# Kernel optimization log

Hardware: AMD Instinct MI355X
Metric: run time of the kernel (lower is better)

The kernel has to match this reference:

```python
import jax, jax.numpy as jnp
import numpy as np

LN_EPS = 1e-5
LOG_EPS = 1e-8

def _layernorm(x, w, b):
    mu = jnp.mean(x, axis=-1, keepdims=True)
    var = jnp.mean((x - mu) ** 2, axis=-1, keepdims=True)
    return (x - mu) * jax.lax.rsqrt(var + LN_EPS) * w + b


def setup_inputs() -> dict:
    key = jax.random.key(0)
    ks = jax.random.split(key, 8)
    B, T, D = 4, 4096, 1024
    x = jax.random.normal(ks[0], (B, T, D), dtype=jnp.float32)
    ln_w = jnp.ones((D,), jnp.float32)
    ln_b = jnp.zeros((D,), jnp.float32)
    # torch Linear stores weight as (out, in)
    Wf = jax.random.normal(ks[1], (D, D), jnp.float32) / np.sqrt(D)
    bf = jax.random.normal(ks[2], (D,), jnp.float32) * 0.02
    # module inits reach to zeros; use small random values for a non-trivial baseline
    Wr = jax.random.normal(ks[3], (D, D), jnp.float32) * 0.02
    br = jax.random.normal(ks[4], (D,), jnp.float32) * 0.02
    alpha_bias = jnp.array([3.0], jnp.float32) + jax.random.normal(ks[5], (1,), jnp.float32) * 0.1
    beta_scale = jnp.array([0.02], jnp.float32)
    return {"x": x, "ln_w": ln_w, "ln_b": ln_b, "Wf": Wf, "bf": bf,
            "Wr": Wr, "br": br, "alpha_bias": alpha_bias, "beta_scale": beta_scale}


def reference(x, ln_w, ln_b, Wf, bf, Wr, br, alpha_bias, beta_scale):
    residual = x
    x_norm = _layernorm(x, ln_w, ln_b)                       # [B,T,D]
    alpha = jax.nn.sigmoid(jnp.einsum('btd,ed->bte', x_norm, Wf) + bf + alpha_bias)
    beta_x = beta_scale * (1.0 - alpha) * x_norm
    log_alpha = jnp.log(alpha + LOG_EPS)
    log_alpha_cumsum = jnp.cumsum(log_alpha, axis=1)          # [B,T,D]
    m = jnp.max(log_alpha_cumsum, axis=1, keepdims=True)      # [B,1,D]
    scale = jnp.exp(log_alpha_cumsum - m)
    x_star = beta_x * scale
    s_star = jnp.cumsum(x_star, axis=1)
    output = s_star / (scale + LOG_EPS)
    x_gate = jnp.tanh(jnp.einsum('btd,ed->bte', output, Wr) + br)
    return x_gate * 0.05 + residual
```

## Files before the change

### kernel.cpp

```cpp
#include <hip/hip_runtime.h>

#define D_DIM 1024
#define B_DIM 4
#define T_DIM 4096
#define M_DIM (B_DIM * T_DIM)
#define CHUNK 32
#define NCHUNK (T_DIM / CHUNK)
#define NWAVE_C 16
#define SEG (NCHUNK / NWAVE_C)

typedef unsigned short u16;
typedef __attribute__((ext_vector_type(8))) __bf16 bf16x8;
typedef __attribute__((ext_vector_type(4))) float f32x4;

__device__ __forceinline__ float bf2f(u16 u) {
    union { unsigned int i; float f; } v;
    v.i = ((unsigned int)u) << 16;
    return v.f;
}
__device__ __forceinline__ u16 f2bf(float f) {
    union { float f; unsigned int i; } v;
    v.f = f;
    unsigned int u = v.i;
    unsigned int r = (u + 0x7fffu + ((u >> 16) & 1u)) >> 16;
    return (u16)r;
}
__device__ __forceinline__ float fast_tanh(float v) {
    float e = __expf(2.f * v);
    return 1.f - 2.f / (e + 1.f);
}

#define GLOAD16(g, l)                                                   \
    __builtin_amdgcn_global_load_lds(                                   \
        (const __attribute__((address_space(1))) void*)(g),             \
        (__attribute__((address_space(3))) void*)(l), 16, 0, 0)

__global__ __launch_bounds__(256) void ln_conv_kernel(const float* __restrict__ x,
                                                      const float* __restrict__ w,
                                                      const float* __restrict__ b,
                                                      u16* __restrict__ xn,
                                                      const float* __restrict__ Wf,
                                                      const float* __restrict__ Wr,
                                                      u16* __restrict__ da,
                                                      u16* __restrict__ db) {
    int tid = threadIdx.x;
    if (blockIdx.x < 2048) {
        int i = blockIdx.x * 256 + tid;
        const float* s = (i < 262144) ? Wf : Wr;
        u16* dp = (i < 262144) ? da : db;
        int j = i & 262143;
        float4 v = ((const float4*)s)[j];
        ushort4 o;
        o.x = f2bf(v.x); o.y = f2bf(v.y); o.z = f2bf(v.z); o.w = f2bf(v.w);
        ((ushort4*)dp)[j] = o;
        return;
    }
    int wv = tid >> 6, lane = tid & 63;
    int row = (blockIdx.x - 2048) * 4 + wv;
    const float4* xr = (const float4*)(x + (size_t)row * D_DIM);
    float4 xv[4];
    #pragma unroll
    for (int k = 0; k < 4; k++) xv[k] = xr[lane + 64 * k];
    float s = 0.f, s2 = 0.f;
    #pragma unroll
    for (int k = 0; k < 4; k++) {
        s  += xv[k].x + xv[k].y + xv[k].z + xv[k].w;
        s2 += xv[k].x * xv[k].x + xv[k].y * xv[k].y
            + xv[k].z * xv[k].z + xv[k].w * xv[k].w;
    }
    #pragma unroll
    for (int o = 1; o < 64; o <<= 1) {
        s  += __shfl_xor(s, o, 64);
        s2 += __shfl_xor(s2, o, 64);
    }
    float mu = s * (1.0f / D_DIM);
    float var = s2 * (1.0f / D_DIM) - mu * mu;
    float rs = rsqrtf(var + 1e-5f);
    ushort4* xo = (ushort4*)(xn + (size_t)row * D_DIM);
    #pragma unroll
    for (int k = 0; k < 4; k++) {
        float4 wv4 = ((const float4*)w)[lane + 64 * k];
        float4 bv4 = ((const float4*)b)[lane + 64 * k];
        ushort4 o;
        o.x = f2bf((xv[k].x - mu) * rs * wv4.x + bv4.x);
        o.y = f2bf((xv[k].y - mu) * rs * wv4.y + bv4.y);
        o.z = f2bf((xv[k].z - mu) * rs * wv4.z + bv4.z);
        o.w = f2bf((xv[k].w - mu) * rs * wv4.w + bv4.w);
        xo[lane + 64 * k] = o;
    }
}

__global__ __launch_bounds__(256) void gemm1_kernel(const u16* __restrict__ xn,
                                                    const u16* __restrict__ Wfc,
                                                    const float* __restrict__ bf_,
                                                    const float* __restrict__ ab,
                                                    const float* __restrict__ bs,
                                                    u16* __restrict__ out_la,
                                                    float* __restrict__ Sg,
                                                    float* __restrict__ Tg) {
    __shared__ __align__(16) u16 lds_a[128 * 32];
    __shared__ __align__(16) u16 lds_b[128 * 32];
    int tid  = threadIdx.x;
    int wave = tid >> 6, lane = tid & 63;
    int tile_n = blockIdx.x * 128;
    int tile_m = blockIdx.y * 128;
    int wr = wave >> 1, wc = wave & 1;
    f32x4 acc[4][4] = {};

    int srow = wave * 32 + (lane >> 2);
    int scol = (lane & 3) * 8;
    const u16* ga0 = xn  + (size_t)(tile_m + srow) * D_DIM + scol;
    const u16* ga1 = ga0 + 16 * D_DIM;
    const u16* gb0 = Wfc + (size_t)(tile_n + srow) * D_DIM + scol;
    const u16* gb1 = gb0 + 16 * D_DIM;
    u16* la0 = &lds_a[(wave * 32) * 32];
    u16* la1 = &lds_a[(wave * 32 + 16) * 32];
    u16* lb0 = &lds_b[(wave * 32) * 32];
    u16* lb1 = &lds_b[(wave * 32 + 16) * 32];

    for (int k0 = 0; k0 < D_DIM; k0 += 32) {
        GLOAD16(ga0 + k0, la0);
        GLOAD16(ga1 + k0, la1);
        GLOAD16(gb0 + k0, lb0);
        GLOAD16(gb1 + k0, lb1);
        __syncthreads();
        bf16x8 af[4], bfr[4];
        #pragma unroll
        for (int mi = 0; mi < 4; mi++) {
            int m = wr * 64 + mi * 16 + (lane & 15);
            af[mi] = *(const bf16x8*)&lds_a[m * 32 + (lane >> 4) * 8];
        }
        #pragma unroll
        for (int ni = 0; ni < 4; ni++) {
            int n = wc * 64 + ni * 16 + (lane & 15);
            bfr[ni] = *(const bf16x8*)&lds_b[n * 32 + (lane >> 4) * 8];
        }
        #pragma unroll
        for (int mi = 0; mi < 4; mi++)
            #pragma unroll
            for (int ni = 0; ni < 4; ni++)
                acc[mi][ni] = __builtin_amdgcn_mfma_f32_16x16x32_bf16(
                    af[mi], bfr[ni], acc[mi][ni], 0, 0, 0);
        __syncthreads();
    }

    float abv = ab[0], bsv = bs[0];
    int q = lane >> 4, l = lane & 15;
    #pragma unroll
    for (int ni = 0; ni < 4; ni++) {
        int col = tile_n + wc * 64 + ni * 16 + l;
        float bcol = bf_[col];
        #pragma unroll
        for (int ch = 0; ch < 2; ch++) {
            float lav[2][4], bxv[2][4];
            #pragma unroll
            for (int h = 0; h < 2; h++) {
                int mi = 2 * ch + h;
                #pragma unroll
                for (int r = 0; r < 4; r++) {
                    int row = tile_m + wr * 64 + mi * 16 + q * 4 + r;
                    float z = acc[mi][ni][r] + bcol + abv;
                    float alpha = 1.f / (1.f + __expf(-z));
                    float la_ = __logf(alpha + 1e-8f);
                    float xv = bf2f(xn[(size_t)row * D_DIM + col]);
                    lav[h][r] = la_;
                    bxv[h][r] = bsv * (1.f - alpha) * xv;
                    out_la[(size_t)row * D_DIM + col] = f2bf(la_);
                }
            }
            float s0 = lav[0][0] + lav[0][1] + lav[0][2] + lav[0][3];
            float s1 = lav[1][0] + lav[1][1] + lav[1][2] + lav[1][3];
            float x0 = s0, x1 = s1, y;
            y = __shfl_up(x0, 16, 64); if (q >= 1) x0 += y;
            y = __shfl_up(x0, 32, 64); if (q >= 2) x0 += y;
            y = __shfl_up(x1, 16, 64); if (q >= 1) x1 += y;
            y = __shfl_up(x1, 32, 64); if (q >= 2) x1 += y;
            float t0 = __shfl(x0, l + 48, 64);
            float t1 = __shfl(x1, l + 48, 64);
            float e0 = x0 - s0, e1 = x1 - s1;
            float pr = e0, Tp = 0.f;
            #pragma unroll
            for (int r = 0; r < 4; r++) { pr += lav[0][r]; Tp += bxv[0][r] * __expf(pr); }
            pr = t0 + e1;
            #pragma unroll
            for (int r = 0; r < 4; r++) { pr += lav[1][r]; Tp += bxv[1][r] * __expf(pr); }
            Tp += __shfl_xor(Tp, 16, 64);
            Tp += __shfl_xor(Tp, 32, 64);
            if (q == 0) {
                int cidx = (tile_m >> 5) + wr * 2 + ch;
                Sg[(size_t)cidx * D_DIM + col] = t0 + t1;
                Tg[(size_t)cidx * D_DIM + col] = Tp;
            }
        }
    }
}

__global__ __launch_bounds__(1024) void scan_combine(const u16* __restrict__ la,
                                                     const float* __restrict__ S,
                                                     const float* __restrict__ Tb,
                                                     float* __restrict__ Of,
                                                     float* __restrict__ SSp) {
    __shared__ float lsS[NWAVE_C][64], lsW[NWAVE_C][64];
    int b = blockIdx.x >> 4;
    int dg = blockIdx.x & 15;
    int wave = threadIdx.x >> 6, lane = threadIdx.x & 63;
    int d = dg * 64 + lane;
    float m = bf2f(la[(size_t)(b * T_DIM) * D_DIM + d]);
    size_t base = ((size_t)b * NCHUNK) * D_DIM + d;
    int c0 = wave * SEG;

    float OfR[SEG], wR[SEG];
    float Or = 0.f, w = 0.f;
    #pragma unroll
    for (int j = 0; j < SEG; j++) {
        size_t ci = base + (size_t)(c0 + j) * D_DIM;
        OfR[j] = Or;
        wR[j]  = w;
        w  += __expf(Or) * Tb[ci];
        Or += S[ci];
    }
    lsS[wave][lane] = Or; lsW[wave][lane] = w;
    __syncthreads();

    float o = 0.f, s = 0.f, myO = 0.f, myS = 0.f;
    #pragma unroll
    for (int w2 = 0; w2 < NWAVE_C; w2++) {
        if (w2 == wave) { myO = o; myS = s; }
        s += __expf(o - m) * lsW[w2][lane];
        o += lsS[w2][lane];
    }

    float em = __expf(myO - m);
    #pragma unroll
    for (int j = 0; j < SEG; j++) {
        size_t ci = base + (size_t)(c0 + j) * D_DIM;
        Of[ci]  = myO + OfR[j] - m;
        SSp[ci] = myS + em * wR[j];
    }
}

__global__ __launch_bounds__(256) void scan_final(const u16* __restrict__ la,
                                                  const u16* __restrict__ xn,
                                                  const float* __restrict__ bs,
                                                  const float* __restrict__ Of,
                                                  const float* __restrict__ SSp,
                                                  u16* __restrict__ osc) {
    int bc = blockIdx.x;
    int b = bc >> 7, c = bc & (NCHUNK - 1);
    int col0 = threadIdx.x * 4;
    float bsv = bs[0];
    size_t base = ((size_t)(b * T_DIM + c * CHUNK)) * D_DIM + col0;
    size_t ci = ((size_t)(b * NCHUNK + c)) * D_DIM + col0;
    float ofs[4], ss[4], p[4];
    #pragma unroll
    for (int j = 0; j < 4; j++) { ofs[j] = Of[ci + j]; ss[j] = SSp[ci + j]; p[j] = 0.f; }
    #pragma unroll 8
    for (int t = 0; t < CHUNK; t++) {
        size_t idx = base + (size_t)t * D_DIM;
        ushort4 lv = *(const ushort4*)(la + idx);
        ushort4 xv = *(const ushort4*)(xn + idx);
        u16 lvs[4] = {lv.x, lv.y, lv.z, lv.w};
        u16 xvs[4] = {xv.x, xv.y, xv.z, xv.w};
        u16 os[4];
        #pragma unroll
        for (int j = 0; j < 4; j++) {
            float lav = bf2f(lvs[j]);
            p[j] += lav;
            float scv = __expf(ofs[j] + p[j]);
            float bx = bsv * (1.f - __expf(lav)) * bf2f(xvs[j]);
            ss[j] += bx * scv;
            os[j] = f2bf(ss[j] / (scv + 1e-8f));
        }
        ushort4 o; o.x = os[0]; o.y = os[1]; o.z = os[2]; o.w = os[3];
        *(ushort4*)(osc + idx) = o;
    }
}

__global__ __launch_bounds__(256) void gemm2_kernel(const u16* __restrict__ A,
                                                    const u16* __restrict__ Bm,
                                                    const float* __restrict__ bias,
                                                    const float* __restrict__ resid,
                                                    float* __restrict__ out_f) {
    __shared__ __align__(16) u16 lds_a[128 * 32];
    __shared__ __align__(16) u16 lds_b[128 * 32];
    int tid  = threadIdx.x;
    int wave = tid >> 6, lane = tid & 63;
    int tile_n = blockIdx.x * 128;
    int tile_m = blockIdx.y * 128;
    int wr = wave >> 1, wc = wave & 1;
    f32x4 acc[4][4] = {};
    int srow = wave * 32 + (lane >> 2);
    int scol = (lane & 3) * 8;
    const u16* ga0 = A  + (size_t)(tile_m + srow) * D_DIM + scol;
    const u16* ga1 = ga0 + 16 * D_DIM;
    const u16* gb0 = Bm + (size_t)(tile_n + srow) * D_DIM + scol;
    const u16* gb1 = gb0 + 16 * D_DIM;
    u16* la0 = &lds_a[(wave * 32) * 32];
    u16* la1 = &lds_a[(wave * 32 + 16) * 32];
    u16* lb0 = &lds_b[(wave * 32) * 32];
    u16* lb1 = &lds_b[(wave * 32 + 16) * 32];
    for (int k0 = 0; k0 < D_DIM; k0 += 32) {
        GLOAD16(ga0 + k0, la0);
        GLOAD16(ga1 + k0, la1);
        GLOAD16(gb0 + k0, lb0);
        GLOAD16(gb1 + k0, lb1);
        __syncthreads();
        bf16x8 af[4], bfr[4];
        #pragma unroll
        for (int mi = 0; mi < 4; mi++) {
            int m = wr * 64 + mi * 16 + (lane & 15);
            af[mi] = *(const bf16x8*)&lds_a[m * 32 + (lane >> 4) * 8];
        }
        #pragma unroll
        for (int ni = 0; ni < 4; ni++) {
            int n = wc * 64 + ni * 16 + (lane & 15);
            bfr[ni] = *(const bf16x8*)&lds_b[n * 32 + (lane >> 4) * 8];
        }
        #pragma unroll
        for (int mi = 0; mi < 4; mi++)
            #pragma unroll
            for (int ni = 0; ni < 4; ni++)
                acc[mi][ni] = __builtin_amdgcn_mfma_f32_16x16x32_bf16(
                    af[mi], bfr[ni], acc[mi][ni], 0, 0, 0);
        __syncthreads();
    }
    #pragma unroll
    for (int mi = 0; mi < 4; mi++) {
        #pragma unroll
        for (int r = 0; r < 4; r++) {
            int row = tile_m + wr * 64 + mi * 16 + (lane >> 4) * 4 + r;
            #pragma unroll
            for (int ni = 0; ni < 4; ni++) {
                int col = tile_n + wc * 64 + ni * 16 + (lane & 15);
                size_t idx = (size_t)row * D_DIM + col;
                float g = fast_tanh(acc[mi][ni][r] + bias[col]);
                out_f[idx] = 0.05f * g + resid[idx];
            }
        }
    }
}

extern "C" void kernel_launch(void* const* d_in, const int* in_sizes, int n_in,
                              void* d_out, int out_size, void* d_ws, size_t ws_size,
                              hipStream_t stream) {
    const float* x   = (const float*)d_in[0];
    const float* lnw = (const float*)d_in[1];
    const float* lnb = (const float*)d_in[2];
    const float* Wf  = (const float*)d_in[3];
    const float* bf_ = (const float*)d_in[4];
    const float* Wr  = (const float*)d_in[5];
    const float* br  = (const float*)d_in[6];
    const float* ab  = (const float*)d_in[7];
    const float* bs  = (const float*)d_in[8];
    float* out = (float*)d_out;

    char* w = (char*)d_ws;
    u16* xn  = (u16*)w;
    u16* la  = (u16*)(w + (size_t)33554432);
    u16* Wfc = (u16*)(w + (size_t)67108864);
    u16* Wrc = (u16*)(w + (size_t)69206016);
    float* S   = (float*)(w + (size_t)71303168);
    float* Tb  = S  + 524288;
    float* Of  = Tb + 524288;
    float* SSp = Of + 524288;
    u16* osc = xn;

    ln_conv_kernel<<<dim3(2048 + M_DIM / 4), dim3(256), 0, stream>>>(
        x, lnw, lnb, xn, Wf, Wr, Wfc, Wrc);
    gemm1_kernel<<<dim3(D_DIM / 128, M_DIM / 128), dim3(256), 0, stream>>>(
        xn, Wfc, bf_, ab, bs, la, S, Tb);
    scan_combine<<<dim3(B_DIM * 16), dim3(1024), 0, stream>>>(la, S, Tb, Of, SSp);
    scan_final<<<dim3(B_DIM * NCHUNK), dim3(256), 0, stream>>>(la, xn, bs, Of, SSp, osc);
    gemm2_kernel<<<dim3(D_DIM / 128, M_DIM / 128), dim3(256), 0, stream>>>(
        osc, Wrc, br, x, out);
}
```

Before: 293.8 us.

## Double-buffer LDS staging in both GEMMs and remap blocks per XCD

Both GEMM kernels now use two LDS buffers so the global-to-LDS loads for the next K-slice are issued while MFMAs run on the current slice, halving the barriers per K step. Block indices are also remapped so each XCD gets a contiguous band of M tiles covering all N tiles, which should improve L2 reuse of the A rows. LDS use per block doubles, which may lower occupancy, and the remap assumes an 8-wide by 128-tall grid.

```diff
diff --git a/kernel.cpp b/kernel.cpp
--- a/kernel.cpp
+++ b/kernel.cpp
@@ -98,12 +98,14 @@
                                                     u16* __restrict__ out_la,
                                                     float* __restrict__ Sg,
                                                     float* __restrict__ Tg) {
-    __shared__ __align__(16) u16 lds_a[128 * 32];
-    __shared__ __align__(16) u16 lds_b[128 * 32];
+    __shared__ __align__(16) u16 lds_a[2][128 * 32];
+    __shared__ __align__(16) u16 lds_b[2][128 * 32];
     int tid  = threadIdx.x;
     int wave = tid >> 6, lane = tid & 63;
-    int tile_n = blockIdx.x * 128;
-    int tile_m = blockIdx.y * 128;
+    int flat = blockIdx.y * 8 + blockIdx.x;
+    int xcd = flat & 7, p = flat >> 3;
+    int tile_m = (xcd * 16 + (p >> 3)) * 128;
+    int tile_n = (p & 7) * 128;
     int wr = wave >> 1, wc = wave & 1;
     f32x4 acc[4][4] = {};
 
@@ -113,36 +115,46 @@
     const u16* ga1 = ga0 + 16 * D_DIM;
     const u16* gb0 = Wfc + (size_t)(tile_n + srow) * D_DIM + scol;
     const u16* gb1 = gb0 + 16 * D_DIM;
-    u16* la0 = &lds_a[(wave * 32) * 32];
-    u16* la1 = &lds_a[(wave * 32 + 16) * 32];
-    u16* lb0 = &lds_b[(wave * 32) * 32];
-    u16* lb1 = &lds_b[(wave * 32 + 16) * 32];
-
-    for (int k0 = 0; k0 < D_DIM; k0 += 32) {
-        GLOAD16(ga0 + k0, la0);
-        GLOAD16(ga1 + k0, la1);
-        GLOAD16(gb0 + k0, lb0);
-        GLOAD16(gb1 + k0, lb1);
+    u16* lA0 = &lds_a[0][(wave * 32) * 32];
+    u16* lA1 = &lds_a[0][(wave * 32 + 16) * 32];
+    u16* lB0 = &lds_b[0][(wave * 32) * 32];
+    u16* lB1 = &lds_b[0][(wave * 32 + 16) * 32];
+
+#define STAGE_G(bufi, kk)                         \
+    do {                                          \
+        GLOAD16(ga0 + (kk), lA0 + (bufi) * 4096); \
+        GLOAD16(ga1 + (kk), lA1 + (bufi) * 4096); \
+        GLOAD16(gb0 + (kk), lB0 + (bufi) * 4096); \
+        GLOAD16(gb1 + (kk), lB1 + (bufi) * 4096); \
+    } while (0)
+
+#define COMPUTE_G(bufi)                                                                      \
+    do {                                                                                     \
+        bf16x8 af[4], bfr[4];                                                                \
+        _Pragma("unroll") for (int mi = 0; mi < 4; mi++)                                     \
+            af[mi] = *(const bf16x8*)&lds_a[bufi][(wr * 64 + mi * 16 + (lane & 15)) * 32 +   \
+                                                  (lane >> 4) * 8];                          \
+        _Pragma("unroll") for (int ni = 0; ni < 4; ni++)                                     \
+            bfr[ni] = *(const bf16x8*)&lds_b[bufi][(wc * 64 + ni * 16 + (lane & 15)) * 32 +  \
+                                                   (lane >> 4) * 8];                         \
+        _Pragma("unroll") for (int mi = 0; mi < 4; mi++)                                     \
+            _Pragma("unroll") for (int ni = 0; ni < 4; ni++)                                 \
+                acc[mi][ni] = __builtin_amdgcn_mfma_f32_16x16x32_bf16(                       \
+                    af[mi], bfr[ni], acc[mi][ni], 0, 0, 0);                                  \
+    } while (0)
+
+    STAGE_G(0, 0);
+    __syncthreads();
+    for (int k0 = 0; k0 < D_DIM; k0 += 64) {
+        STAGE_G(1, k0 + 32);
+        COMPUTE_G(0);
         __syncthreads();
-        bf16x8 af[4], bfr[4];
-        #pragma unroll
-        for (int mi = 0; mi < 4; mi++) {
-            int m = wr * 64 + mi * 16 + (lane & 15);
-            af[mi] = *(const bf16x8*)&lds_a[m * 32 + (lane >> 4) * 8];
-        }
-        #pragma unroll
-        for (int ni = 0; ni < 4; ni++) {
-            int n = wc * 64 + ni * 16 + (lane & 15);
-            bfr[ni] = *(const bf16x8*)&lds_b[n * 32 + (lane >> 4) * 8];
-        }
-        #pragma unroll
-        for (int mi = 0; mi < 4; mi++)
-            #pragma unroll
-            for (int ni = 0; ni < 4; ni++)
-                acc[mi][ni] = __builtin_amdgcn_mfma_f32_16x16x32_bf16(
-                    af[mi], bfr[ni], acc[mi][ni], 0, 0, 0);
+        if (k0 + 64 < D_DIM) STAGE_G(0, k0 + 64);
+        COMPUTE_G(1);
         __syncthreads();
     }
+#undef STAGE_G
+#undef COMPUTE_G
 
     float abv = ab[0], bsv = bs[0];
     int q = lane >> 4, l = lane & 15;
@@ -281,12 +293,14 @@
                                                     const float* __restrict__ bias,
                                                     const float* __restrict__ resid,
                                                     float* __restrict__ out_f) {
-    __shared__ __align__(16) u16 lds_a[128 * 32];
-    __shared__ __align__(16) u16 lds_b[128 * 32];
+    __shared__ __align__(16) u16 lds_a[2][128 * 32];
+    __shared__ __align__(16) u16 lds_b[2][128 * 32];
     int tid  = threadIdx.x;
     int wave = tid >> 6, lane = tid & 63;
-    int tile_n = blockIdx.x * 128;
-    int tile_m = blockIdx.y * 128;
+    int flat = blockIdx.y * 8 + blockIdx.x;
+    int xcd = flat & 7, p = flat >> 3;
+    int tile_m = (xcd * 16 + (p >> 3)) * 128;
+    int tile_n = (p & 7) * 128;
     int wr = wave >> 1, wc = wave & 1;
     f32x4 acc[4][4] = {};
     int srow = wave * 32 + (lane >> 2);
@@ -295,35 +309,47 @@
     const u16* ga1 = ga0 + 16 * D_DIM;
     const u16* gb0 = Bm + (size_t)(tile_n + srow) * D_DIM + scol;
     const u16* gb1 = gb0 + 16 * D_DIM;
-    u16* la0 = &lds_a[(wave * 32) * 32];
-    u16* la1 = &lds_a[(wave * 32 + 16) * 32];
-    u16* lb0 = &lds_b[(wave * 32) * 32];
-    u16* lb1 = &lds_b[(wave * 32 + 16) * 32];
-    for (int k0 = 0; k0 < D_DIM; k0 += 32) {
-        GLOAD16(ga0 + k0, la0);
-        GLOAD16(ga1 + k0, la1);
-        GLOAD16(gb0 + k0, lb0);
-        GLOAD16(gb1 + k0, lb1);
+    u16* lA0 = &lds_a[0][(wave * 32) * 32];
+    u16* lA1 = &lds_a[0][(wave * 32 + 16) * 32];
+    u16* lB0 = &lds_b[0][(wave * 32) * 32];
+    u16* lB1 = &lds_b[0][(wave * 32 + 16) * 32];
+
+#define STAGE_G(bufi, kk)                         \
+    do {                                          \
+        GLOAD16(ga0 + (kk), lA0 + (bufi) * 4096); \
+        GLOAD16(ga1 + (kk), lA1 + (bufi) * 4096); \
+        GLOAD16(gb0 + (kk), lB0 + (bufi) * 4096); \
+        GLOAD16(gb1 + (kk), lB1 + (bufi) * 4096); \
+    } while (0)
+
+#define COMPUTE_G(bufi)                                                                      \
+    do {                                                                                     \
+        bf16x8 af[4], bfr[4];                                                                \
+        _Pragma("unroll") for (int mi = 0; mi < 4; mi++)                                     \
+            af[mi] = *(const bf16x8*)&lds_a[bufi][(wr * 64 + mi * 16 + (lane & 15)) * 32 +   \
+                                                  (lane >> 4) * 8];                          \
+        _Pragma("unroll") for (int ni = 0; ni < 4; ni++)                                     \
+            bfr[ni] = *(const bf16x8*)&lds_b[bufi][(wc * 64 + ni * 16 + (lane & 15)) * 32 +  \
+                                                   (lane >> 4) * 8];                         \
+        _Pragma("unroll") for (int mi = 0; mi < 4; mi++)                                     \
+            _Pragma("unroll") for (int ni = 0; ni < 4; ni++)                                 \
+                acc[mi][ni] = __builtin_amdgcn_mfma_f32_16x16x32_bf16(                       \
+                    af[mi], bfr[ni], acc[mi][ni], 0, 0, 0);                                  \
+    } while (0)
+
+    STAGE_G(0, 0);
+    __syncthreads();
+    for (int k0 = 0; k0 < D_DIM; k0 += 64) {
+        STAGE_G(1, k0 + 32);
+        COMPUTE_G(0);
         __syncthreads();
-        bf16x8 af[4], bfr[4];
-        #pragma unroll
-        for (int mi = 0; mi < 4; mi++) {
-            int m = wr * 64 + mi * 16 + (lane & 15);
-            af[mi] = *(const bf16x8*)&lds_a[m * 32 + (lane >> 4) * 8];
-        }
-        #pragma unroll
-        for (int ni = 0; ni < 4; ni++) {
-            int n = wc * 64 + ni * 16 + (lane & 15);
-            bfr[ni] = *(const bf16x8*)&lds_b[n * 32 + (lane >> 4) * 8];
-        }
-        #pragma unroll
-        for (int mi = 0; mi < 4; mi++)
-            #pragma unroll
-            for (int ni = 0; ni < 4; ni++)
-                acc[mi][ni] = __builtin_amdgcn_mfma_f32_16x16x32_bf16(
-                    af[mi], bfr[ni], acc[mi][ni], 0, 0, 0);
+        if (k0 + 64 < D_DIM) STAGE_G(0, k0 + 64);
+        COMPUTE_G(1);
         __syncthreads();
     }
+#undef STAGE_G
+#undef COMPUTE_G
+
     #pragma unroll
     for (int mi = 0; mi < 4; mi++) {
         #pragma unroll
```

New measurement: 295.7 us. Within noise of the previous version (+0.7%).

## Rewrite both GEMMs with 256x256 tiles, double-buffered swizzled LDS and XCD-aware mapping

Applied to the files above, without the earlier changes.

Both GEMM kernels now share a core that uses 256x256 output tiles with 512 threads and a 64-wide K step. Global-to-LDS loads are double-buffered with explicit vmcnt waits and barriers, the LDS layout is XOR-swizzled to avoid bank conflicts, and MFMA batches run at raised priority. Blocks are remapped so neighbouring tiles land on the same XCD for L2 reuse. The aim is higher MFMA utilisation and less load latency exposure, at the cost of more registers and LDS per block (128KB), which lowers occupancy and leaves only 256 blocks per GEMM.

```diff
diff --git a/kernel.cpp b/kernel.cpp
--- a/kernel.cpp
+++ b/kernel.cpp
@@ -8,6 +8,7 @@
 #define NCHUNK (T_DIM / CHUNK)
 #define NWAVE_C 16
 #define SEG (NCHUNK / NWAVE_C)
+#define NKT (D_DIM / 64)
 
 typedef unsigned short u16;
 typedef __attribute__((ext_vector_type(8))) __bf16 bf16x8;
@@ -34,6 +35,17 @@
     __builtin_amdgcn_global_load_lds(                                   \
         (const __attribute__((address_space(1))) void*)(g),             \
         (__attribute__((address_space(3))) void*)(l), 16, 0, 0)
+
+#define BAR()                                      \
+    do {                                           \
+        __builtin_amdgcn_sched_barrier(0);         \
+        asm volatile("" ::: "memory");             \
+        __builtin_amdgcn_s_barrier();              \
+        asm volatile("" ::: "memory");             \
+        __builtin_amdgcn_sched_barrier(0);         \
+    } while (0)
+
+#define WAITVM(N) asm volatile("s_waitcnt vmcnt(" #N ")" ::: "memory")
 
 __global__ __launch_bounds__(256) void ln_conv_kernel(const float* __restrict__ x,
                                                       const float* __restrict__ w,
@@ -90,60 +102,119 @@
     }
 }
 
-__global__ __launch_bounds__(256) void gemm1_kernel(const u16* __restrict__ xn,
-                                                    const u16* __restrict__ Wfc,
-                                                    const float* __restrict__ bf_,
-                                                    const float* __restrict__ ab,
-                                                    const float* __restrict__ bs,
-                                                    u16* __restrict__ out_la,
-                                                    float* __restrict__ Sg,
-                                                    float* __restrict__ Tg) {
-    __shared__ __align__(16) u16 lds_a[128 * 32];
-    __shared__ __align__(16) u16 lds_b[128 * 32];
+__device__ __forceinline__ void gemm256_core(const u16* __restrict__ AG,
+                                             const u16* __restrict__ BG,
+                                             int tile_m, int tile_n,
+                                             u16* ldsA, u16* ldsB,
+                                             f32x4 (*acc)[4]) {
     int tid  = threadIdx.x;
     int wave = tid >> 6, lane = tid & 63;
-    int tile_n = blockIdx.x * 128;
-    int tile_m = blockIdx.y * 128;
-    int wr = wave >> 1, wc = wave & 1;
-    f32x4 acc[4][4] = {};
-
-    int srow = wave * 32 + (lane >> 2);
-    int scol = (lane & 3) * 8;
-    const u16* ga0 = xn  + (size_t)(tile_m + srow) * D_DIM + scol;
-    const u16* ga1 = ga0 + 16 * D_DIM;
-    const u16* gb0 = Wfc + (size_t)(tile_n + srow) * D_DIM + scol;
-    const u16* gb1 = gb0 + 16 * D_DIM;
-    u16* la0 = &lds_a[(wave * 32) * 32];
-    u16* la1 = &lds_a[(wave * 32 + 16) * 32];
-    u16* lb0 = &lds_b[(wave * 32) * 32];
-    u16* lb1 = &lds_b[(wave * 32 + 16) * 32];
-
-    for (int k0 = 0; k0 < D_DIM; k0 += 32) {
-        GLOAD16(ga0 + k0, la0);
-        GLOAD16(ga1 + k0, la1);
-        GLOAD16(gb0 + k0, lb0);
-        GLOAD16(gb1 + k0, lb1);
-        __syncthreads();
-        bf16x8 af[4], bfr[4];
+    int wr = wave >> 2, wc = wave & 3;
+    int q = lane >> 4;
+    int srow = tid >> 3;
+    int scol = ((tid & 7) ^ (srow & 7)) * 8;
+    const u16* gA = AG + (size_t)(tile_m + srow) * D_DIM + scol;
+    const u16* gB = BG + (size_t)(tile_n + srow) * D_DIM + scol;
+    int ldst = wave * 512;
+    int aRow = wr * 128 + (lane & 15);
+    int bRow = wc * 64 + (lane & 15);
+    int x7 = lane & 7;
+    int s0 = (q ^ x7) * 8;
+    int s1 = ((4 | q) ^ x7) * 8;
+
+#define STG4(ldsbase, gsrc, koff)                                        \
+    do {                                                                 \
+        _Pragma("unroll") for (int j = 0; j < 4; j++)                    \
+            GLOAD16((gsrc) + (size_t)j * (64 * D_DIM) + (koff),          \
+                    (ldsbase) + j * 4096 + ldst);                        \
+    } while (0)
+
+#define MMQ(Af, Bf, mo, no)                                              \
+    do {                                                                 \
+        __builtin_amdgcn_s_setprio(1);                                   \
+        _Pragma("unroll") for (int mi_ = 0; mi_ < 4; mi_++)              \
+            _Pragma("unroll") for (int ni_ = 0; ni_ < 2; ni_++) {        \
+                acc[(mo) + mi_][(no) + ni_] =                            \
+                    __builtin_amdgcn_mfma_f32_16x16x32_bf16(             \
+                        Af[mi_][0], Bf[ni_][0],                          \
+                        acc[(mo) + mi_][(no) + ni_], 0, 0, 0);           \
+                acc[(mo) + mi_][(no) + ni_] =                            \
+                    __builtin_amdgcn_mfma_f32_16x16x32_bf16(             \
+                        Af[mi_][1], Bf[ni_][1],                          \
+                        acc[(mo) + mi_][(no) + ni_], 0, 0, 0);           \
+            }                                                            \
+        __builtin_amdgcn_s_setprio(0);                                   \
+    } while (0)
+
+    STG4(ldsA, gA, 0);
+    STG4(ldsB, gB, 0);
+    STG4(ldsA + 16384, gA, 64);
+    STG4(ldsB + 16384, gB, 64);
+    WAITVM(8);
+    BAR();
+
+    for (int t = 0; t < NKT; t++) {
+        int c = t & 1;
+        const u16* pA = ldsA + c * 16384 + aRow * 64;
+        const u16* pB = ldsB + c * 16384 + bRow * 64;
+        bf16x8 A0[4][2], A1[4][2], B0[2][2], B1[2][2];
         #pragma unroll
         for (int mi = 0; mi < 4; mi++) {
-            int m = wr * 64 + mi * 16 + (lane & 15);
-            af[mi] = *(const bf16x8*)&lds_a[m * 32 + (lane >> 4) * 8];
-        }
-        #pragma unroll
-        for (int ni = 0; ni < 4; ni++) {
-            int n = wc * 64 + ni * 16 + (lane & 15);
-            bfr[ni] = *(const bf16x8*)&lds_b[n * 32 + (lane >> 4) * 8];
-        }
-        #pragma unroll
-        for (int mi = 0; mi < 4; mi++)
-            #pragma unroll
-            for (int ni = 0; ni < 4; ni++)
-                acc[mi][ni] = __builtin_amdgcn_mfma_f32_16x16x32_bf16(
-                    af[mi], bfr[ni], acc[mi][ni], 0, 0, 0);
-        __syncthreads();
-    }
-
+            A0[mi][0] = *(const bf16x8*)(pA + mi * 1024 + s0);
+            A0[mi][1] = *(const bf16x8*)(pA + mi * 1024 + s1);
+        }
+        #pragma unroll
+        for (int ni = 0; ni < 2; ni++) {
+            B0[ni][0] = *(const bf16x8*)(pB + ni * 1024 + s0);
+            B0[ni][1] = *(const bf16x8*)(pB + ni * 1024 + s1);
+        }
+        MMQ(A0, B0, 0, 0);
+        #pragma unroll
+        for (int mi = 0; mi < 4; mi++) {
+            A1[mi][0] = *(const bf16x8*)(pA + (mi + 4) * 1024 + s0);
+            A1[mi][1] = *(const bf16x8*)(pA + (mi + 4) * 1024 + s1);
+        }
+        #pragma unroll
+        for (int ni = 0; ni < 2; ni++) {
+            B1[ni][0] = *(const bf16x8*)(pB + (ni + 2) * 1024 + s0);
+            B1[ni][1] = *(const bf16x8*)(pB + (ni + 2) * 1024 + s1);
+        }
+        MMQ(A0, B1, 0, 2);
+        BAR();
+        if (t + 2 < NKT) STG4(ldsA + c * 16384, gA, (size_t)(t + 2) * 64);
+        MMQ(A1, B0, 4, 0);
+        if (t + 2 < NKT) {
+            STG4(ldsB + c * 16384, gB, (size_t)(t + 2) * 64);
+            WAITVM(8);
+        } else {
+            WAITVM(0);
+        }
+        BAR();
+        MMQ(A1, B1, 4, 2);
+    }
+#undef STG4
+#undef MMQ
+}
+
+__global__ __launch_bounds__(512, 2) void gemm1_kernel(const u16* __restrict__ xn,
+                                                       const u16* __restrict__ Wfc,
+                                                       const float* __restrict__ bf_,
+                                                       const float* __restrict__ ab,
+                                                       const float* __restrict__ bs,
+                                                       u16* __restrict__ out_la,
+                                                       float* __restrict__ Sg,
+                                                       float* __restrict__ Tg) {
+    __shared__ __align__(16) u16 ldsA[2][16384];
+    __shared__ __align__(16) u16 ldsB[2][16384];
+    int flat = blockIdx.y * 4 + blockIdx.x;
+    int xcd = flat & 7, p = flat >> 3;
+    int tile_m = (xcd * 8 + (p >> 2)) * 256;
+    int tile_n = (p & 3) * 256;
+    f32x4 acc[8][4] = {};
+    gemm256_core(xn, Wfc, tile_m, tile_n, &ldsA[0][0], &ldsB[0][0], acc);
+
+    int tid = threadIdx.x, wave = tid >> 6, lane = tid & 63;
+    int wr = wave >> 2, wc = wave & 3;
     float abv = ab[0], bsv = bs[0];
     int q = lane >> 4, l = lane & 15;
     #pragma unroll
@@ -151,14 +222,14 @@
         int col = tile_n + wc * 64 + ni * 16 + l;
         float bcol = bf_[col];
         #pragma unroll
-        for (int ch = 0; ch < 2; ch++) {
+        for (int ch = 0; ch < 4; ch++) {
             float lav[2][4], bxv[2][4];
             #pragma unroll
             for (int h = 0; h < 2; h++) {
                 int mi = 2 * ch + h;
                 #pragma unroll
                 for (int r = 0; r < 4; r++) {
-                    int row = tile_m + wr * 64 + mi * 16 + q * 4 + r;
+                    int row = tile_m + wr * 128 + mi * 16 + q * 4 + r;
                     float z = acc[mi][ni][r] + bcol + abv;
                     float alpha = 1.f / (1.f + __expf(-z));
                     float la_ = __logf(alpha + 1e-8f);
@@ -187,7 +258,7 @@
             Tp += __shfl_xor(Tp, 16, 64);
             Tp += __shfl_xor(Tp, 32, 64);
             if (q == 0) {
-                int cidx = (tile_m >> 5) + wr * 2 + ch;
+                int cidx = ((tile_m + wr * 128) >> 5) + ch;
                 Sg[(size_t)cidx * D_DIM + col] = t0 + t1;
                 Tg[(size_t)cidx * D_DIM + col] = Tp;
             }
@@ -276,62 +347,31 @@
     }
 }
 
-__global__ __launch_bounds__(256) void gemm2_kernel(const u16* __restrict__ A,
-                                                    const u16* __restrict__ Bm,
-                                                    const float* __restrict__ bias,
-                                                    const float* __restrict__ resid,
-                                                    float* __restrict__ out_f) {
-    __shared__ __align__(16) u16 lds_a[128 * 32];
-    __shared__ __align__(16) u16 lds_b[128 * 32];
-    int tid  = threadIdx.x;
-    int wave = tid >> 6, lane = tid & 63;
-    int tile_n = blockIdx.x * 128;
-    int tile_m = blockIdx.y * 128;
-    int wr = wave >> 1, wc = wave & 1;
-    f32x4 acc[4][4] = {};
-    int srow = wave * 32 + (lane >> 2);
-    int scol = (lane & 3) * 8;
-    const u16* ga0 = A  + (size_t)(tile_m + srow) * D_DIM + scol;
-    const u16* ga1 = ga0 + 16 * D_DIM;
-    const u16* gb0 = Bm + (size_t)(tile_n + srow) * D_DIM + scol;
-    const u16* gb1 = gb0 + 16 * D_DIM;
-    u16* la0 = &lds_a[(wave * 32) * 32];
-    u16* la1 = &lds_a[(wave * 32 + 16) * 32];
-    u16* lb0 = &lds_b[(wave * 32) * 32];
-    u16* lb1 = &lds_b[(wave * 32 + 16) * 32];
-    for (int k0 = 0; k0 < D_DIM; k0 += 32) {
-        GLOAD16(ga0 + k0, la0);
-        GLOAD16(ga1 + k0, la1);
-        GLOAD16(gb0 + k0, lb0);
-        GLOAD16(gb1 + k0, lb1);
-        __syncthreads();
-        bf16x8 af[4], bfr[4];
-        #pragma unroll
-        for (int mi = 0; mi < 4; mi++) {
-            int m = wr * 64 + mi * 16 + (lane & 15);
-            af[mi] = *(const bf16x8*)&lds_a[m * 32 + (lane >> 4) * 8];
-        }
-        #pragma unroll
-        for (int ni = 0; ni < 4; ni++) {
-            int n = wc * 64 + ni * 16 + (lane & 15);
-            bfr[ni] = *(const bf16x8*)&lds_b[n * 32 + (lane >> 4) * 8];
-        }
-        #pragma unroll
-        for (int mi = 0; mi < 4; mi++)
-            #pragma unroll
-            for (int ni = 0; ni < 4; ni++)
-                acc[mi][ni] = __builtin_amdgcn_mfma_f32_16x16x32_bf16(
-                    af[mi], bfr[ni], acc[mi][ni], 0, 0, 0);
-        __syncthreads();
-    }
-    #pragma unroll
-    for (int mi = 0; mi < 4; mi++) {
+__global__ __launch_bounds__(512, 2) void gemm2_kernel(const u16* __restrict__ A,
+                                                       const u16* __restrict__ Bm,
+                                                       const float* __restrict__ bias,
+                                                       const float* __restrict__ resid,
+                                                       float* __restrict__ out_f) {
+    __shared__ __align__(16) u16 ldsA[2][16384];
+    __shared__ __align__(16) u16 ldsB[2][16384];
+    int flat = blockIdx.y * 4 + blockIdx.x;
+    int xcd = flat & 7, p = flat >> 3;
+    int tile_m = (xcd * 8 + (p >> 2)) * 256;
+    int tile_n = (p & 3) * 256;
+    f32x4 acc[8][4] = {};
+    gemm256_core(A, Bm, tile_m, tile_n, &ldsA[0][0], &ldsB[0][0], acc);
+
+    int tid = threadIdx.x, wave = tid >> 6, lane = tid & 63;
+    int wr = wave >> 2, wc = wave & 3;
+    int q = lane >> 4, l = lane & 15;
+    #pragma unroll
+    for (int mi = 0; mi < 8; mi++) {
         #pragma unroll
         for (int r = 0; r < 4; r++) {
-            int row = tile_m + wr * 64 + mi * 16 + (lane >> 4) * 4 + r;
+            int row = tile_m + wr * 128 + mi * 16 + q * 4 + r;
             #pragma unroll
             for (int ni = 0; ni < 4; ni++) {
-                int col = tile_n + wc * 64 + ni * 16 + (lane & 15);
+                int col = tile_n + wc * 64 + ni * 16 + l;
                 size_t idx = (size_t)row * D_DIM + col;
                 float g = fast_tanh(acc[mi][ni][r] + bias[col]);
                 out_f[idx] = 0.05f * g + resid[idx];
@@ -367,10 +407,10 @@
 
     ln_conv_kernel<<<dim3(2048 + M_DIM / 4), dim3(256), 0, stream>>>(
         x, lnw, lnb, xn, Wf, Wr, Wfc, Wrc);
-    gemm1_kernel<<<dim3(D_DIM / 128, M_DIM / 128), dim3(256), 0, stream>>>(
+    gemm1_kernel<<<dim3(D_DIM / 256, M_DIM / 256), dim3(512), 0, stream>>>(
         xn, Wfc, bf_, ab, bs, la, S, Tb);
     scan_combine<<<dim3(B_DIM * 16), dim3(1024), 0, stream>>>(la, S, Tb, Of, SSp);
     scan_final<<<dim3(B_DIM * NCHUNK), dim3(256), 0, stream>>>(la, xn, bs, Of, SSp, osc);
-    gemm2_kernel<<<dim3(D_DIM / 128, M_DIM / 128), dim3(256), 0, stream>>>(
+    gemm2_kernel<<<dim3(D_DIM / 256, M_DIM / 256), dim3(512), 0, stream>>>(
         osc, Wrc, br, x, out);
 }
```

Measured after the change: 274.0 us. 6.7% less time.
